# Kernel optimization log

Measured on AMD Instinct MI355X. Metric: run time of the kernel, lower is better.

Reference implementation:

```python
import jax, jax.numpy as jnp
import numpy as np

TGT_NUM = 256  # init kwarg tgt_num


def setup_inputs() -> dict:
    key = jax.random.key(0)
    k1, k2 = jax.random.split(key)
    B, L, D = 64, 4096, 256
    video_feats = jax.random.normal(k1, (B, L, D), dtype=jnp.float32)
    video_masks = jax.random.randint(k2, (B, L), 0, 2).astype(bool)
    # guarantee at least one valid frame per video (torch code assumes src_num >= 1)
    video_masks = video_masks.at[:, 0].set(True)
    return {"video_feats": video_feats, "video_masks": video_masks}


def _aggregate_one(feats, mask, tgt_num):
    # feats: [L, D], mask: [L] bool
    L, D = feats.shape
    n = mask.sum()  # src_num (traced int)
    # compact valid frames to the front (equivalent of feats[mask]); OOB scatter
    # indices (== L) are dropped by default in jax scatters.
    cidx = jnp.cumsum(mask) - 1
    safe_idx = jnp.where(mask, cidx, L)
    comp = jnp.zeros_like(feats).at[safe_idx].set(feats)  # [L, D], valid rows first
    # bucket boundaries: round(k / tgt_num * n), clamped to n - 1  (round-half-even,
    # matching torch.round / jnp.round)
    k = jnp.arange(tgt_num + 1, dtype=jnp.float32)
    nf = n.astype(jnp.float32)
    idxs = jnp.minimum(jnp.round(k / tgt_num * nf), nf - 1.0).astype(jnp.int32)  # [T+1]
    s, e = idxs[:-1], idxs[1:]  # [T]
    j = jnp.arange(L, dtype=jnp.int32)[None, :]  # [1, L]
    in_range = (j >= s[:, None]) & (j < e[:, None])  # [T, L]
    denom = jnp.maximum(e - s, 1).astype(feats.dtype)  # avoid div-by-zero when s >= e
    mean_w = in_range.astype(feats.dtype) / denom[:, None]
    single_w = (j == s[:, None]).astype(feats.dtype)  # bucket is single row s when s >= e
    w = jnp.where((s < e)[:, None], mean_w, single_w)  # [T, L]
    return w @ comp  # [T, D]


def reference(video_feats, video_masks):
    agg = lambda f, m: _aggregate_one(f, m, TGT_NUM)
    return jax.vmap(agg)(video_feats, video_masks)  # [B, T, D]
```

## Files before the change

kernel.cpp:

```cpp
#include <hip/hip_runtime.h>
#include <stdint.h>

#define B_DIM 64
#define L_DIM 4096
#define D_DIM 256
#define TGT 256
#define NG 32
#define ROWS_PER_BLOCK (TGT / NG)

__device__ __forceinline__ int idx_of(int k, float nf) {
    float x = rintf((float)k * (1.0f / 256.0f) * nf);
    x = fminf(x, nf - 1.0f);
    return (int)x;
}

__global__ __launch_bounds__(256)
void AggregateVideo_kernel(const uint8_t* __restrict__ mask_raw,
                           const float* __restrict__ feats,
                           float* __restrict__ out) {
    __shared__ unsigned short pos[L_DIM];
    __shared__ int tsum[256];
    __shared__ int flags[2];

    const int tid = threadIdx.x;
    const int b   = blockIdx.y;
    const int g   = blockIdx.x;

    if (tid == 0) { flags[0] = 1; flags[1] = 1; }
    __syncthreads();
    {
        const uint32_t* mw = (const uint32_t*)mask_raw;
        bool bad_int = false, bad_f32 = false;
        #pragma unroll
        for (int i = 0; i < 4; ++i) {
            uint32_t w = mw[tid + 256 * i];
            if (w > 1u) bad_int = true;
            if (w != 0u && w != 0x3F800000u) bad_f32 = true;
        }
        if (bad_int) flags[0] = 0;
        if (bad_f32) flags[1] = 0;
    }
    __syncthreads();
    const int flag = flags[0] ? 1 : (flags[1] ? 2 : 0);

    uint32_t bits = 0;
    int cnt = 0;
    {
        const int base = tid * 16;
        if (flag == 1) {
            const int32_t* m = (const int32_t*)mask_raw + (size_t)b * L_DIM;
            #pragma unroll
            for (int i = 0; i < 16; ++i)
                if (m[base + i] != 0) { bits |= (1u << i); ++cnt; }
        } else if (flag == 2) {
            const float* m = (const float*)mask_raw + (size_t)b * L_DIM;
            #pragma unroll
            for (int i = 0; i < 16; ++i)
                if (m[base + i] != 0.0f) { bits |= (1u << i); ++cnt; }
        } else {
            const uint8_t* m = mask_raw + (size_t)b * L_DIM;
            #pragma unroll
            for (int i = 0; i < 16; ++i)
                if (m[base + i] != 0) { bits |= (1u << i); ++cnt; }
        }
    }
    tsum[tid] = cnt;
    __syncthreads();
    for (int off = 1; off < 256; off <<= 1) {
        int v = (tid >= off) ? tsum[tid - off] : 0;
        __syncthreads();
        tsum[tid] += v;
        __syncthreads();
    }
    const int n = tsum[255];
    {
        int p = tsum[tid] - cnt;
        const int base = tid * 16;
        #pragma unroll
        for (int i = 0; i < 16; ++i)
            if ((bits >> i) & 1u) pos[p++] = (unsigned short)(base + i);
    }
    __syncthreads();

    const float nf = (float)n;

    const int wv   = tid >> 6;
    const int lane = tid & 63;
    for (int r = wv; r < ROWS_PER_BLOCK; r += 4) {
        const int t = g * ROWS_PER_BLOCK + r;
        const int s = idx_of(t, nf);
        const int e = idx_of(t + 1, nf);
        const int lo = s;
        const int hi = (e > s) ? e : (s + 1);
        const float inv = 1.0f / (float)(hi - lo);
        float4 acc = make_float4(0.f, 0.f, 0.f, 0.f);
        for (int i = lo; i < hi; ++i) {
            const int row = pos[i];
            const float4 v =
                *((const float4*)(feats + ((size_t)b * L_DIM + row) * D_DIM) + lane);
            acc.x += v.x; acc.y += v.y; acc.z += v.z; acc.w += v.w;
        }
        acc.x *= inv; acc.y *= inv; acc.z *= inv; acc.w *= inv;
        *((float4*)(out + ((size_t)b * TGT + t) * D_DIM) + lane) = acc;
    }
}

extern "C" void kernel_launch(void* const* d_in, const int* in_sizes, int n_in,
                              void* d_out, int out_size, void* d_ws, size_t ws_size,
                              hipStream_t stream) {
    const float*   feats = (const float*)d_in[0];
    const uint8_t* masks = (const uint8_t*)d_in[1];
    float*         out   = (float*)d_out;
    (void)in_sizes; (void)n_in; (void)out_size; (void)d_ws; (void)ws_size;

    dim3 grid(NG, B_DIM);
    AggregateVideo_kernel<<<grid, 256, 0, stream>>>(masks, feats, out);
}
```

Measured before the change: 30.86 us.

## Split mask compaction into a separate kernel to avoid redundant per-block scans

The mask scan and compaction now run once per batch in a dedicated kernel that writes positions and counts to workspace. A second gather kernel reads them instead of each of the 32 blocks per batch redoing the scan. This removes 32x redundant mask reads and prefix sums, at the cost of an extra kernel launch and a global round-trip for the position array. The old fused kernel is kept as a fallback when the workspace is too small.

Measured after the change: 32.39 us. 1.05x slower.

```diff
diff --git a/kernel.cpp b/kernel.cpp
--- a/kernel.cpp
+++ b/kernel.cpp
@@ -15,16 +15,13 @@
 }
 
 __global__ __launch_bounds__(256)
-void AggregateVideo_kernel(const uint8_t* __restrict__ mask_raw,
-                           const float* __restrict__ feats,
-                           float* __restrict__ out) {
-    __shared__ unsigned short pos[L_DIM];
+void build_pos_kernel(const uint8_t* __restrict__ mask_raw,
+                      unsigned short* __restrict__ pos_ws,
+                      int* __restrict__ n_ws) {
     __shared__ int tsum[256];
     __shared__ int flags[2];
-
     const int tid = threadIdx.x;
-    const int b   = blockIdx.y;
-    const int g   = blockIdx.x;
+    const int b   = blockIdx.x;
 
     if (tid == 0) { flags[0] = 1; flags[1] = 1; }
     __syncthreads();
@@ -72,18 +69,119 @@
         tsum[tid] += v;
         __syncthreads();
     }
-    const int n = tsum[255];
     {
         int p = tsum[tid] - cnt;
         const int base = tid * 16;
+        unsigned short* pos = pos_ws + (size_t)b * L_DIM;
         #pragma unroll
         for (int i = 0; i < 16; ++i)
             if ((bits >> i) & 1u) pos[p++] = (unsigned short)(base + i);
     }
+    if (tid == 255) n_ws[b] = tsum[255];
+}
+
+__global__ __launch_bounds__(256)
+void gather_kernel(const float* __restrict__ feats,
+                   const unsigned short* __restrict__ pos_ws,
+                   const int* __restrict__ n_ws,
+                   float* __restrict__ out) {
+    const int tid  = threadIdx.x;
+    const int b    = blockIdx.y;
+    const int g    = blockIdx.x;
+    const int wv   = tid >> 6;
+    const int lane = tid & 63;
+
+    const float nf = (float)n_ws[b];
+    const unsigned short* pos = pos_ws + (size_t)b * L_DIM;
+    const float* fb = feats + (size_t)b * L_DIM * D_DIM;
+
+    for (int r = wv; r < ROWS_PER_BLOCK; r += 4) {
+        const int t  = g * ROWS_PER_BLOCK + r;
+        const int s  = idx_of(t, nf);
+        const int e  = idx_of(t + 1, nf);
+        const int lo = s;
+        const int hi = (e > s) ? e : (s + 1);
+        const float inv = 1.0f / (float)(hi - lo);
+        float4 acc = make_float4(0.f, 0.f, 0.f, 0.f);
+        for (int i = lo; i < hi; ++i) {
+            const int row = pos[i];
+            const float4 v = *((const float4*)(fb + (size_t)row * D_DIM) + lane);
+            acc.x += v.x; acc.y += v.y; acc.z += v.z; acc.w += v.w;
+        }
+        acc.x *= inv; acc.y *= inv; acc.z *= inv; acc.w *= inv;
+        *((float4*)(out + ((size_t)b * TGT + t) * D_DIM) + lane) = acc;
+    }
+}
+
+__global__ __launch_bounds__(256)
+void AggregateVideo_fused_kernel(const uint8_t* __restrict__ mask_raw,
+                                 const float* __restrict__ feats,
+                                 float* __restrict__ out) {
+    __shared__ unsigned short pos[L_DIM];
+    __shared__ int tsum[256];
+    __shared__ int flags[2];
+
+    const int tid = threadIdx.x;
+    const int b   = blockIdx.y;
+    const int g   = blockIdx.x;
+
+    if (tid == 0) { flags[0] = 1; flags[1] = 1; }
+    __syncthreads();
+    {
+        const uint32_t* mw = (const uint32_t*)mask_raw;
+        bool bad_int = false, bad_f32 = false;
+        #pragma unroll
+        for (int i = 0; i < 4; ++i) {
+            uint32_t w = mw[tid + 256 * i];
+            if (w > 1u) bad_int = true;
+            if (w != 0u && w != 0x3F800000u) bad_f32 = true;
+        }
+        if (bad_int) flags[0] = 0;
+        if (bad_f32) flags[1] = 0;
+    }
+    __syncthreads();
+    const int flag = flags[0] ? 1 : (flags[1] ? 2 : 0);
+
+    uint32_t bits = 0;
+    int cnt = 0;
+    {
+        const int base = tid * 16;
+        if (flag == 1) {
+            const int32_t* m = (const int32_t*)mask_raw + (size_t)b * L_DIM;
+            #pragma unroll
+            for (int i = 0; i < 16; ++i)
+                if (m[base + i] != 0) { bits |= (1u << i); ++cnt; }
+        } else if (flag == 2) {
+            const float* m = (const float*)mask_raw + (size_t)b * L_DIM;
+            #pragma unroll
+            for (int i = 0; i < 16; ++i)
+                if (m[base + i] != 0.0f) { bits |= (1u << i); ++cnt; }
+        } else {
+            const uint8_t* m = mask_raw + (size_t)b * L_DIM;
+            #pragma unroll
+            for (int i = 0; i < 16; ++i)
+                if (m[base + i] != 0) { bits |= (1u << i); ++cnt; }
+        }
+    }
+    tsum[tid] = cnt;
+    __syncthreads();
+    for (int off = 1; off < 256; off <<= 1) {
+        int v = (tid >= off) ? tsum[tid - off] : 0;
+        __syncthreads();
+        tsum[tid] += v;
+        __syncthreads();
+    }
+    const int n = tsum[255];
+    {
+        int p = tsum[tid] - cnt;
+        const int base = tid * 16;
+        #pragma unroll
+        for (int i = 0; i < 16; ++i)
+            if ((bits >> i) & 1u) pos[p++] = (unsigned short)(base + i);
+    }
     __syncthreads();
 
     const float nf = (float)n;
-
     const int wv   = tid >> 6;
     const int lane = tid & 63;
     for (int r = wv; r < ROWS_PER_BLOCK; r += 4) {
@@ -111,8 +209,19 @@
     const float*   feats = (const float*)d_in[0];
     const uint8_t* masks = (const uint8_t*)d_in[1];
     float*         out   = (float*)d_out;
-    (void)in_sizes; (void)n_in; (void)out_size; (void)d_ws; (void)ws_size;
-
-    dim3 grid(NG, B_DIM);
-    AggregateVideo_kernel<<<grid, 256, 0, stream>>>(masks, feats, out);
-}
+    (void)in_sizes; (void)n_in; (void)out_size;
+
+    const size_t pos_bytes = (size_t)B_DIM * L_DIM * sizeof(unsigned short);
+    const size_t need      = pos_bytes + B_DIM * sizeof(int);
+
+    if (ws_size >= need) {
+        unsigned short* pos_ws = (unsigned short*)d_ws;
+        int*            n_ws   = (int*)((uint8_t*)d_ws + pos_bytes);
+        build_pos_kernel<<<B_DIM, 256, 0, stream>>>(masks, pos_ws, n_ws);
+        dim3 grid(NG, B_DIM);
+        gather_kernel<<<grid, 256, 0, stream>>>(feats, pos_ws, n_ws, out);
+    } else {
+        dim3 grid(NG, B_DIM);
+        AggregateVideo_fused_kernel<<<grid, 256, 0, stream>>>(masks, feats, out);
+    }
+}
```

## Use ballot-based mask compaction, larger blocks, and unrolled gather accumulation

Applied to the files above, without the earlier changes.

Replaces the per-thread 16-bit mask scan and 8-step shared-memory prefix sum with wavefront ballots into 64-bit words, a single-wave shuffle scan over the word popcounts, and byte-wise bit extraction to build the compacted position list. Blocks grow to 512 threads and each block handles 16 output rows, so half as many blocks redo the per-video mask compaction. The gather loop broadcasts row indices by shuffle and keeps four independent accumulators so more loads are in flight. It assumes a bucket holds at most 64 rows, which holds here because n is at most 4096 and there are 256 buckets. Summation order also changes slightly.

Result: slower. 31.71 us (+2.7%).

```diff
diff --git a/kernel.cpp b/kernel.cpp
--- a/kernel.cpp
+++ b/kernel.cpp
@@ -5,8 +5,9 @@
 #define L_DIM 4096
 #define D_DIM 256
 #define TGT 256
-#define NG 32
-#define ROWS_PER_BLOCK (TGT / NG)
+#define BLK 512
+#define ROWS_PER_BLOCK 16
+#define NG (TGT / ROWS_PER_BLOCK)
 
 __device__ __forceinline__ int idx_of(int k, float nf) {
     float x = rintf((float)k * (1.0f / 256.0f) * nf);
@@ -14,17 +15,21 @@
     return (int)x;
 }
 
-__global__ __launch_bounds__(256)
+__global__ __launch_bounds__(BLK)
 void AggregateVideo_kernel(const uint8_t* __restrict__ mask_raw,
                            const float* __restrict__ feats,
                            float* __restrict__ out) {
     __shared__ unsigned short pos[L_DIM];
-    __shared__ int tsum[256];
+    __shared__ unsigned long long words[L_DIM / 64];
+    __shared__ int pref[L_DIM / 64];
     __shared__ int flags[2];
+    __shared__ int nsh;
 
-    const int tid = threadIdx.x;
-    const int b   = blockIdx.y;
-    const int g   = blockIdx.x;
+    const int tid  = threadIdx.x;
+    const int b    = blockIdx.y;
+    const int g    = blockIdx.x;
+    const int wv   = tid >> 6;
+    const int lane = tid & 63;
 
     if (tid == 0) { flags[0] = 1; flags[1] = 1; }
     __syncthreads();
@@ -32,8 +37,8 @@
         const uint32_t* mw = (const uint32_t*)mask_raw;
         bool bad_int = false, bad_f32 = false;
         #pragma unroll
-        for (int i = 0; i < 4; ++i) {
-            uint32_t w = mw[tid + 256 * i];
+        for (int i = 0; i < 2; ++i) {
+            uint32_t w = mw[tid + BLK * i];
             if (w > 1u) bad_int = true;
             if (w != 0u && w != 0x3F800000u) bad_f32 = true;
         }
@@ -43,65 +48,110 @@
     __syncthreads();
     const int flag = flags[0] ? 1 : (flags[1] ? 2 : 0);
 
-    uint32_t bits = 0;
-    int cnt = 0;
     {
-        const int base = tid * 16;
         if (flag == 1) {
             const int32_t* m = (const int32_t*)mask_raw + (size_t)b * L_DIM;
             #pragma unroll
-            for (int i = 0; i < 16; ++i)
-                if (m[base + i] != 0) { bits |= (1u << i); ++cnt; }
+            for (int i = 0; i < L_DIM / BLK; ++i) {
+                const int j = i * BLK + tid;
+                unsigned long long bal = __ballot(m[j] != 0);
+                if (lane == 0) words[j >> 6] = bal;
+            }
         } else if (flag == 2) {
             const float* m = (const float*)mask_raw + (size_t)b * L_DIM;
             #pragma unroll
-            for (int i = 0; i < 16; ++i)
-                if (m[base + i] != 0.0f) { bits |= (1u << i); ++cnt; }
+            for (int i = 0; i < L_DIM / BLK; ++i) {
+                const int j = i * BLK + tid;
+                unsigned long long bal = __ballot(m[j] != 0.0f);
+                if (lane == 0) words[j >> 6] = bal;
+            }
         } else {
             const uint8_t* m = mask_raw + (size_t)b * L_DIM;
             #pragma unroll
-            for (int i = 0; i < 16; ++i)
-                if (m[base + i] != 0) { bits |= (1u << i); ++cnt; }
+            for (int i = 0; i < L_DIM / BLK; ++i) {
+                const int j = i * BLK + tid;
+                unsigned long long bal = __ballot(m[j] != 0);
+                if (lane == 0) words[j >> 6] = bal;
+            }
         }
-    }
-    tsum[tid] = cnt;
-    __syncthreads();
-    for (int off = 1; off < 256; off <<= 1) {
-        int v = (tid >= off) ? tsum[tid - off] : 0;
-        __syncthreads();
-        tsum[tid] += v;
-        __syncthreads();
-    }
-    const int n = tsum[255];
-    {
-        int p = tsum[tid] - cnt;
-        const int base = tid * 16;
-        #pragma unroll
-        for (int i = 0; i < 16; ++i)
-            if ((bits >> i) & 1u) pos[p++] = (unsigned short)(base + i);
     }
     __syncthreads();
 
-    const float nf = (float)n;
+    if (tid < 64) {
+        const unsigned long long wd = words[tid];
+        const int c = __popcll(wd);
+        int inc = c;
+        #pragma unroll
+        for (int off = 1; off < 64; off <<= 1) {
+            int v = __shfl_up(inc, off);
+            if (tid >= off) inc += v;
+        }
+        pref[tid] = inc - c;
+        if (tid == 63) nsh = inc;
+    }
+    __syncthreads();
 
-    const int wv   = tid >> 6;
-    const int lane = tid & 63;
-    for (int r = wv; r < ROWS_PER_BLOCK; r += 4) {
-        const int t = g * ROWS_PER_BLOCK + r;
-        const int s = idx_of(t, nf);
-        const int e = idx_of(t + 1, nf);
+    {
+        const int w      = tid >> 3;
+        const int startb = (tid & 7) * 8;
+        const unsigned long long wd = words[w];
+        const unsigned long long below =
+            startb ? (wd & ((1ull << startb) - 1ull)) : 0ull;
+        int p = pref[w] + __popcll(below);
+        const int base = w * 64 + startb;
+        unsigned int byte = (unsigned int)((wd >> startb) & 0xFFull);
+        while (byte) {
+            const int bit = __ffs(byte) - 1;
+            pos[p++] = (unsigned short)(base + bit);
+            byte &= byte - 1;
+        }
+    }
+    __syncthreads();
+
+    const float nf = (float)nsh;
+    const float* fb = feats + (size_t)b * L_DIM * D_DIM;
+
+    #pragma unroll
+    for (int rr = 0; rr < 2; ++rr) {
+        const int t  = g * ROWS_PER_BLOCK + wv + rr * 8;
+        const int s  = idx_of(t, nf);
+        const int e  = idx_of(t + 1, nf);
         const int lo = s;
         const int hi = (e > s) ? e : (s + 1);
-        const float inv = 1.0f / (float)(hi - lo);
-        float4 acc = make_float4(0.f, 0.f, 0.f, 0.f);
-        for (int i = lo; i < hi; ++i) {
-            const int row = pos[i];
-            const float4 v =
-                *((const float4*)(feats + ((size_t)b * L_DIM + row) * D_DIM) + lane);
-            acc.x += v.x; acc.y += v.y; acc.z += v.z; acc.w += v.w;
+        const int cnt = hi - lo;
+        const float inv = 1.0f / (float)cnt;
+
+        const int myrow = (lane < cnt) ? (int)pos[lo + lane] : 0;
+
+        float4 a0 = make_float4(0.f, 0.f, 0.f, 0.f);
+        float4 a1 = make_float4(0.f, 0.f, 0.f, 0.f);
+        float4 a2 = make_float4(0.f, 0.f, 0.f, 0.f);
+        float4 a3 = make_float4(0.f, 0.f, 0.f, 0.f);
+        int k = 0;
+        for (; k + 4 <= cnt; k += 4) {
+            const int r0 = __shfl(myrow, k);
+            const int r1 = __shfl(myrow, k + 1);
+            const int r2 = __shfl(myrow, k + 2);
+            const int r3 = __shfl(myrow, k + 3);
+            const float4 v0 = *((const float4*)(fb + (size_t)r0 * D_DIM) + lane);
+            const float4 v1 = *((const float4*)(fb + (size_t)r1 * D_DIM) + lane);
+            const float4 v2 = *((const float4*)(fb + (size_t)r2 * D_DIM) + lane);
+            const float4 v3 = *((const float4*)(fb + (size_t)r3 * D_DIM) + lane);
+            a0.x += v0.x; a0.y += v0.y; a0.z += v0.z; a0.w += v0.w;
+            a1.x += v1.x; a1.y += v1.y; a1.z += v1.z; a1.w += v1.w;
+            a2.x += v2.x; a2.y += v2.y; a2.z += v2.z; a2.w += v2.w;
+            a3.x += v3.x; a3.y += v3.y; a3.z += v3.z; a3.w += v3.w;
         }
-        acc.x *= inv; acc.y *= inv; acc.z *= inv; acc.w *= inv;
-        *((float4*)(out + ((size_t)b * TGT + t) * D_DIM) + lane) = acc;
+        for (; k < cnt; ++k) {
+            const int r0 = __shfl(myrow, k);
+            const float4 v0 = *((const float4*)(fb + (size_t)r0 * D_DIM) + lane);
+            a0.x += v0.x; a0.y += v0.y; a0.z += v0.z; a0.w += v0.w;
+        }
+        a0.x += a1.x; a0.y += a1.y; a0.z += a1.z; a0.w += a1.w;
+        a2.x += a3.x; a2.y += a3.y; a2.z += a3.z; a2.w += a3.w;
+        a0.x += a2.x; a0.y += a2.y; a0.z += a2.z; a0.w += a2.w;
+        a0.x *= inv; a0.y *= inv; a0.z *= inv; a0.w *= inv;
+        *((float4*)(out + ((size_t)b * TGT + t) * D_DIM) + lane) = a0;
     }
 }
 
@@ -114,5 +164,5 @@
     (void)in_sizes; (void)n_in; (void)out_size; (void)d_ws; (void)ws_size;
 
     dim3 grid(NG, B_DIM);
-    AggregateVideo_kernel<<<grid, 256, 0, stream>>>(masks, feats, out);
+    AggregateVideo_kernel<<<grid, BLK, 0, stream>>>(masks, feats, out);
 }
```
